# Kernel tuning notes

Measured on AMD Instinct MI355X. Metric: run time of the kernel, lower is better.

Reference implementation:

```python
import jax, jax.numpy as jnp
import numpy as np

P = 256          # planes == in_planes
EPS = 1e-5       # BatchNorm eps


def binarize(x):
    # sign with sign(0) -> +1, as in standard binary-net quantizers
    return jnp.where(x >= 0, 1.0, -1.0).astype(x.dtype)


def bin_conv(x, w, stride=1):
    """XNOR-style binarized 3x3 conv: sign(x) * sign(w), scaled by per-out-channel mean |w|."""
    ba = binarize(x)
    bw = binarize(w)
    scale = jnp.mean(jnp.abs(w), axis=(1, 2, 3))  # [O]
    y = jax.lax.conv_general_dilated(
        ba, bw, window_strides=(stride, stride), padding=((1, 1), (1, 1)),
        dimension_numbers=("NCHW", "OIHW", "NCHW"))
    return y * scale[None, :, None, None]


def bn(x, gamma, beta, mean, var):
    # inference-mode BatchNorm2d
    inv = gamma / jnp.sqrt(var + EPS)
    return x * inv[None, :, None, None] + (beta - mean * inv)[None, :, None, None]


def channel_shuffle(x, groups=2):
    b, c, h, w = x.shape
    return x.reshape(b, groups, c // groups, h, w).transpose(0, 2, 1, 3, 4).reshape(b, c, h, w)


def setup_inputs() -> dict:
    key = jax.random.key(0)
    ks = jax.random.split(key, 8)
    B, H, W = 16, 56, 56
    return {
        "x": jax.random.normal(ks[0], (B, 2 * P, H, W), jnp.float32),
        "w1": jax.random.normal(ks[1], (P, P, 3, 3), jnp.float32) * 0.05,
        "w2": jax.random.normal(ks[2], (P, 2 * P, 3, 3), jnp.float32) * 0.05,
        "gamma1": jnp.ones((P,), jnp.float32),
        "beta1": jnp.zeros((P,), jnp.float32),
        "mean1": jax.random.normal(ks[3], (P,), jnp.float32) * 0.1,
        "var1": jax.random.uniform(ks[4], (P,), jnp.float32) + 0.5,
        "gamma2": jnp.ones((P,), jnp.float32),
        "beta2": jnp.zeros((P,), jnp.float32),
        "mean2": jax.random.normal(ks[5], (P,), jnp.float32) * 0.1,
        "var2": jax.random.uniform(ks[6], (P,), jnp.float32) + 0.5,
        "move_bias": jax.random.normal(ks[7], (1, P, 1, 1), jnp.float32) * 0.1,
    }


def reference(x, w1, w2, gamma1, beta1, mean1, var1,
              gamma2, beta2, mean2, var2, move_bias):
    x_act, x_idle = x[:, :P], x[:, P:]
    residual = x_act
    out = bn(bin_conv(x_act, w1, stride=1), gamma1, beta1, mean1, var1)
    out = out + residual
    out = jnp.clip(out, -1.0, 1.0)            # Hardtanh
    x_idle = x_idle + move_bias               # LearnableBias
    out = jnp.concatenate([out, x_idle], axis=1)   # [B, 2P, H, W]
    out = channel_shuffle(out, groups=2)
    residual1 = out[:, :P]
    out = bn(bin_conv(out, w2, stride=1), gamma2, beta2, mean2, var2)
    out = out + residual1
    out = jnp.clip(out, -1.0, 1.0)            # Hardtanh
    return out
```

## Files before the change

### kernel.cpp

```cpp
#include <hip/hip_runtime.h>
#include <cstdint>

typedef unsigned long long u64;
typedef unsigned short u16;

#define HWSZ 3136
#define WD 56
#define NPIX 50176
#define HS 58
#define IMG 3364

__device__ __forceinline__ float clampf(float v){ return fminf(1.0f, fmaxf(-1.0f, v)); }
__device__ __forceinline__ u16 f2bf(float f){
    unsigned u = __float_as_uint(f);
    return (u16)((u + 0x7fffu + ((u >> 16) & 1u)) >> 16);
}
__device__ __forceinline__ float bf2f(u16 h){ return __uint_as_float(((unsigned)h) << 16); }
__device__ __forceinline__ int xp(u64 a, u64 b, int s){
    u64 x = a ^ b;
    s += __popc((unsigned)x);
    s += __popc((unsigned)(x >> 32));
    return s;
}

__device__ __forceinline__ void conv_pass2(
    const u64* __restrict__ bits, const u64* wlds, int colbase,
    int base, int (&accA)[8][2], int (&accB)[8][2])
{
#pragma unroll 1
    for (int dy = -1; dy <= 1; dy++) {
        const ulonglong2* rp = (const ulonglong2*)(bits + (size_t)(base + dy * HS) * 4);
        ulonglong2 plo[4], phi[4];
#pragma unroll
        for (int k = 0; k < 4; k++) { plo[k] = rp[2 * k]; phi[k] = rp[2 * k + 1]; }
#pragma unroll
        for (int dx = 0; dx < 3; dx++) {
            int t = (dy + 1) * 3 + dx;
#pragma unroll
            for (int co = 0; co < 8; co++) {
                const ulonglong2* wp = (const ulonglong2*)&wlds[((colbase + co) * 9 + t) * 4];
                ulonglong2 wA = wp[0], wB = wp[1];
#pragma unroll
                for (int p = 0; p < 2; p++) {
                    int k = dx + p; int s = accA[co][p];
                    s = xp(plo[k].x, wA.x, s); s = xp(plo[k].y, wA.y, s);
                    s = xp(phi[k].x, wB.x, s); s = xp(phi[k].y, wB.y, s);
                    accA[co][p] = s;
                }
            }
#pragma unroll
            for (int co = 0; co < 8; co++) {
                const ulonglong2* wp = (const ulonglong2*)&wlds[((colbase + 8 + co) * 9 + t) * 4];
                ulonglong2 wA = wp[0], wB = wp[1];
#pragma unroll
                for (int p = 0; p < 2; p++) {
                    int k = dx + p; int s = accB[co][p];
                    s = xp(plo[k].x, wA.x, s); s = xp(plo[k].y, wA.y, s);
                    s = xp(phi[k].x, wB.x, s); s = xp(phi[k].y, wB.y, s);
                    accB[co][p] = s;
                }
            }
        }
    }
}

__global__ __launch_bounds__(256) void k_wprep(
    const float* __restrict__ w1, const float* __restrict__ w2,
    const float* __restrict__ g1, const float* __restrict__ be1,
    const float* __restrict__ m1, const float* __restrict__ v1,
    const float* __restrict__ g2, const float* __restrict__ be2,
    const float* __restrict__ m2, const float* __restrict__ v2,
    u64* __restrict__ w1b, u64* __restrict__ w2e, u64* __restrict__ w2o,
    float* __restrict__ A1, float* __restrict__ B1,
    float* __restrict__ A2, float* __restrict__ B2,
    int* __restrict__ C1s, int* __restrict__ C2s)
{
    int co  = blockIdx.x;
    int tid = threadIdx.x;
    int wv = tid >> 6, lane = tid & 63;
    int ci = (wv << 6) + lane;

    __shared__ int spc1[4][9], spc2[4][9];

    float s1 = 0.f, s2 = 0.f;
    const float* w1p = w1 + ((size_t)co * 256 + ci) * 9;
#pragma unroll
    for (int t = 0; t < 9; t++) {
        float v = w1p[t];
        s1 += fabsf(v);
        u64 bal = __ballot(v >= 0.f);
        if (lane == 0) { w1b[(co * 9 + t) * 4 + wv] = bal; spc1[wv][t] = __popcll(bal); }
    }
    const float* wep = w2 + ((size_t)co * 512 + 2 * ci) * 9;
    const float* wop = wep + 9;
#pragma unroll
    for (int t = 0; t < 9; t++) {
        float ve = wep[t], vo = wop[t];
        s2 += fabsf(ve) + fabsf(vo);
        u64 bale = __ballot(ve >= 0.f);
        u64 balo = __ballot(vo >= 0.f);
        if (lane == 0) {
            w2e[(co * 9 + t) * 4 + wv] = bale; w2o[(co * 9 + t) * 4 + wv] = balo;
            spc2[wv][t] = __popcll(bale) + __popcll(balo);
        }
    }
    __shared__ float red1[256], red2[256];
    red1[tid] = s1; red2[tid] = s2;
    __syncthreads();
    for (int off = 128; off > 0; off >>= 1) {
        if (tid < off) { red1[tid] += red1[tid + off]; red2[tid] += red2[tid + off]; }
        __syncthreads();
    }
    if (tid == 0) {
        float scale1 = red1[0] / 2304.f;
        float scale2 = red2[0] / 4608.f;
        float inv1 = g1[co] / sqrtf(v1[co] + 1e-5f);
        float inv2 = g2[co] / sqrtf(v2[co] + 1e-5f);
        A1[co] = scale1 * inv1;  B1[co] = be1[co] - m1[co] * inv1;
        A2[co] = scale2 * inv2;  B2[co] = be2[co] - m2[co] * inv2;
        int pc1[9], pc2[9];
#pragma unroll
        for (int t = 0; t < 9; t++) {
            pc1[t] = spc1[0][t] + spc1[1][t] + spc1[2][t] + spc1[3][t];
            pc2[t] = spc2[0][t] + spc2[1][t] + spc2[2][t] + spc2[3][t];
        }
        int* c1 = C1s + co * 8;
        c1[0] = pc1[0] + pc1[1] + pc1[2];
        c1[1] = pc1[6] + pc1[7] + pc1[8];
        c1[2] = pc1[0] + pc1[3] + pc1[6];
        c1[3] = pc1[2] + pc1[5] + pc1[8];
        c1[4] = pc1[0]; c1[5] = pc1[2]; c1[6] = pc1[6]; c1[7] = pc1[8];
        int* c2 = C2s + co * 8;
        c2[0] = pc2[0] + pc2[1] + pc2[2];
        c2[1] = pc2[6] + pc2[7] + pc2[8];
        c2[2] = pc2[0] + pc2[3] + pc2[6];
        c2[3] = pc2[2] + pc2[5] + pc2[8];
        c2[4] = pc2[0]; c2[5] = pc2[2]; c2[6] = pc2[6]; c2[7] = pc2[8];
    }
}

__global__ __launch_bounds__(256) void k_zero(ulonglong2* __restrict__ dst, int n)
{
    int i = blockIdx.x * 256 + threadIdx.x;
    if (i < n) { ulonglong2 z; z.x = 0; z.y = 0; dst[i] = z; }
}

__global__ __launch_bounds__(256) void k_pack(
    const float* __restrict__ x, const float* __restrict__ mb,
    u64* __restrict__ bitsA, u64* __restrict__ bitsI)
{
    int tid = threadIdx.x;
    int p = blockIdx.x * 256 + tid;
    int q = blockIdx.y;
    int b = p / HWSZ, hw = p % HWSZ;
    int h = hw / WD, w = hw % WD;
    const float* xa = x + ((size_t)(b * 512 + q * 64)) * HWSZ + hw;
    const float* xi = x + ((size_t)(b * 512 + 256 + q * 64)) * HWSZ + hw;
    const float* mbq = mb + q * 64;
    u64 wa = 0, wi = 0;
#pragma unroll 8
    for (int j = 0; j < 64; j++) {
        float va = xa[(size_t)j * HWSZ];
        float vi = xi[(size_t)j * HWSZ] + mbq[j];
        wa |= (u64)(va >= 0.f) << j;
        wi |= (u64)(vi >= 0.f) << j;
    }
    size_t pos = ((size_t)b * IMG + (h + 1) * HS + (w + 1)) * 4 + q;
    bitsA[pos] = wa;
    bitsI[pos] = wi;
}

__global__ __launch_bounds__(256, 4) void k_conv1(
    const float* __restrict__ x, const u64* __restrict__ bitsA,
    const u64* __restrict__ w1b, const float* __restrict__ A1,
    const float* __restrict__ B1, const int* __restrict__ C1s,
    u64* __restrict__ bitsC, u16* __restrict__ c1v)
{
    __shared__ __align__(16) u64 sw[2304];
    __shared__ float sA[64], sB[64];
    __shared__ int scr[512];
    __shared__ u16 spart[4][128];
    int tid = threadIdx.x, q = blockIdx.y, cobase = q * 64;
    {
        const u64* src = w1b + (size_t)cobase * 36;
#pragma unroll
        for (int i = 0; i < 9; i++) sw[tid + i * 256] = src[tid + i * 256];
        if (tid < 64) { sA[tid] = A1[cobase + tid]; sB[tid] = B1[cobase + tid]; }
        scr[tid] = C1s[cobase * 8 + tid];
        scr[tid + 256] = C1s[cobase * 8 + tid + 256];
    }
    __syncthreads();

    int wid = tid >> 6, lane = tid & 63;
    int gu = __builtin_amdgcn_readfirstlane(wid);
    int pix0 = blockIdx.x * 128 + lane * 2;
    int b = pix0 / HWSZ, hw = pix0 % HWSZ, h = hw / WD, w = hw % WD;
    int base = b * IMG + (h + 1) * HS + w;

    int accA[8][2] = {}, accB[8][2] = {};
    conv_pass2(bitsA, sw, gu << 4, base, accA, accB);

    int mt = (h == 0), mbo = (h == WD - 1);
    int wl = (w == 0), wr = (w == 54);
    int nvr = 3 - mt - mbo;
    int nv0 = nvr * (3 - wl), nv1 = nvr * (3 - wr);

    unsigned sb0 = 0, sb1 = 0;
    bool wrv = (q < 2);
#pragma unroll
    for (int half = 0; half < 2; half++)
#pragma unroll
    for (int co = 0; co < 8; co++) {
        int col = (gu << 4) + half * 8 + co;
        int coG = cobase + col, bit = half * 8 + co;
        float A = sA[col], Bc = sB[col];
        const int* cs = &scr[col * 8];
        int a0 = half ? accB[co][0] : accA[co][0];
        int a1 = half ? accB[co][1] : accA[co][1];
        int ctb = (mt ? cs[0] : 0) + (mbo ? cs[1] : 0);
        int corr0 = ctb + (wl ? (cs[2] - (mt ? cs[4] : 0) - (mbo ? cs[6] : 0)) : 0);
        int corr1 = ctb + (wr ? (cs[3] - (mt ? cs[5] : 0) - (mbo ? cs[7] : 0)) : 0);
        float2 xr = *(const float2*)(x + ((size_t)(b * 512 + coG)) * HWSZ + hw);
        float v0 = (float)((nv0 << 8) + 2 * (corr0 - a0)) * A + Bc + xr.x;
        float v1 = (float)((nv1 << 8) + 2 * (corr1 - a1)) * A + Bc + xr.y;
        sb0 |= (unsigned)(v0 >= 0.f) << bit;
        sb1 |= (unsigned)(v1 >= 0.f) << bit;
        if (wrv) {
            ushort2 st; st.x = f2bf(clampf(v0)); st.y = f2bf(clampf(v1));
            *(ushort2*)(c1v + (size_t)coG * NPIX + pix0) = st;
        }
    }
    spart[wid][lane * 2]     = (u16)sb0;
    spart[wid][lane * 2 + 1] = (u16)sb1;
    __syncthreads();
    if (wid == 0) {
#pragma unroll
        for (int p = 0; p < 2; p++) {
            int pi = lane * 2 + p;
            u64 word = (u64)spart[0][pi] | ((u64)spart[1][pi] << 16)
                     | ((u64)spart[2][pi] << 32) | ((u64)spart[3][pi] << 48);
            bitsC[(size_t)(base + 1 + p) * 4 + q] = word;
        }
    }
}

__global__ __launch_bounds__(256, 4) void k_conv2(
    const float* __restrict__ x, const float* __restrict__ mb,
    const u64* __restrict__ bitsC, const u64* __restrict__ bitsI,
    const u64* __restrict__ w2e, const u64* __restrict__ w2o,
    const float* __restrict__ A2, const float* __restrict__ B2,
    const int* __restrict__ C2s,
    const u16* __restrict__ c1v, float* __restrict__ out)
{
    __shared__ __align__(16) u64 se[2304], so[2304];
    __shared__ float sA[64], sB[64], sM[32];
    __shared__ int scr[512];
    int tid = threadIdx.x, q = blockIdx.y, cobase = q * 64;
    {
        const u64* srcE = w2e + (size_t)cobase * 36;
        const u64* srcO = w2o + (size_t)cobase * 36;
#pragma unroll
        for (int i = 0; i < 9; i++) { se[tid + i * 256] = srcE[tid + i * 256]; so[tid + i * 256] = srcO[tid + i * 256]; }
        if (tid < 64) { sA[tid] = A2[cobase + tid]; sB[tid] = B2[cobase + tid]; }
        if (tid >= 64 && tid < 96) sM[tid - 64] = mb[q * 32 + tid - 64];
        scr[tid] = C2s[cobase * 8 + tid];
        scr[tid + 256] = C2s[cobase * 8 + tid + 256];
    }
    __syncthreads();

    int wid = tid >> 6, lane = tid & 63;
    int gu = __builtin_amdgcn_readfirstlane(wid);
    int pix0 = blockIdx.x * 128 + lane * 2;
    int b = pix0 / HWSZ, hw = pix0 % HWSZ, h = hw / WD, w = hw % WD;
    int base = b * IMG + (h + 1) * HS + w;

    int accA[8][2] = {}, accB[8][2] = {};
    conv_pass2(bitsC, se, gu << 4, base, accA, accB);
    conv_pass2(bitsI, so, gu << 4, base, accA, accB);

    int mt = (h == 0), mbo = (h == WD - 1);
    int wl = (w == 0), wr = (w == 54);
    int nvr = 3 - mt - mbo;
    int nv0 = nvr * (3 - wl), nv1 = nvr * (3 - wr);

#pragma unroll
    for (int half = 0; half < 2; half++)
#pragma unroll
    for (int co = 0; co < 8; co++) {
        int col = (gu << 4) + half * 8 + co;
        int coG = cobase + col, cg2 = coG >> 1;
        float A = sA[col], Bc = sB[col];
        const int* cs = &scr[col * 8];
        int a0 = half ? accB[co][0] : accA[co][0];
        int a1 = half ? accB[co][1] : accA[co][1];
        int ctb = (mt ? cs[0] : 0) + (mbo ? cs[1] : 0);
        int corr0 = ctb + (wl ? (cs[2] - (mt ? cs[4] : 0) - (mbo ? cs[6] : 0)) : 0);
        int corr1 = ctb + (wr ? (cs[3] - (mt ? cs[5] : 0) - (mbo ? cs[7] : 0)) : 0);
        float r0, r1;
        if ((co & 1) == 0) {
            ushort2 cv = *(const ushort2*)(c1v + (size_t)cg2 * NPIX + pix0);
            r0 = bf2f(cv.x); r1 = bf2f(cv.y);
        } else {
            float2 xi = *(const float2*)(x + ((size_t)(b * 512 + 256 + cg2)) * HWSZ + hw);
            float mv = sM[col >> 1];
            r0 = xi.x + mv; r1 = xi.y + mv;
        }
        float2 ov;
        ov.x = clampf((float)((nv0 << 9) + 2 * (corr0 - a0)) * A + Bc + r0);
        ov.y = clampf((float)((nv1 << 9) + 2 * (corr1 - a1)) * A + Bc + r1);
        *(float2*)(out + ((size_t)(b * 256 + coG)) * HWSZ + hw) = ov;
    }
}

extern "C" void kernel_launch(void* const* d_in, const int* in_sizes, int n_in,
                              void* d_out, int out_size, void* d_ws, size_t ws_size,
                              hipStream_t stream)
{
    const float* x   = (const float*)d_in[0];
    const float* w1  = (const float*)d_in[1];
    const float* w2  = (const float*)d_in[2];
    const float* g1  = (const float*)d_in[3];
    const float* be1 = (const float*)d_in[4];
    const float* m1  = (const float*)d_in[5];
    const float* v1  = (const float*)d_in[6];
    const float* g2  = (const float*)d_in[7];
    const float* be2 = (const float*)d_in[8];
    const float* m2  = (const float*)d_in[9];
    const float* v2  = (const float*)d_in[10];
    const float* mb  = (const float*)d_in[11];

    char* ws = (char*)d_ws;
    u64* w1b = (u64*)ws; ws += 73728;
    u64* w2e = (u64*)ws; ws += 73728;
    u64* w2o = (u64*)ws; ws += 73728;
    float* A1 = (float*)ws; ws += 1024;
    float* B1 = (float*)ws; ws += 1024;
    float* A2 = (float*)ws; ws += 1024;
    float* B2 = (float*)ws; ws += 1024;
    int* C1s = (int*)ws; ws += 8192;
    int* C2s = (int*)ws; ws += 8192;
    u64* bitsA = (u64*)ws; ws += (size_t)16 * IMG * 4 * 8;
    u64* bitsI = (u64*)ws; ws += (size_t)16 * IMG * 4 * 8;
    u64* bitsC = (u64*)ws; ws += (size_t)16 * IMG * 4 * 8;
    u16* c1v = (u16*)ws; ws += (size_t)128 * NPIX * 2;

    int nzero2 = (int)(3 * (size_t)16 * IMG * 4 * 8 / 16);

    hipLaunchKernelGGL(k_wprep, dim3(256), dim3(256), 0, stream,
                       w1, w2, g1, be1, m1, v1, g2, be2, m2, v2,
                       w1b, w2e, w2o, A1, B1, A2, B2, C1s, C2s);
    hipLaunchKernelGGL(k_zero, dim3((nzero2 + 255) / 256), dim3(256), 0, stream,
                       (ulonglong2*)bitsA, nzero2);
    hipLaunchKernelGGL(k_pack, dim3(196, 4), dim3(256), 0, stream, x, mb, bitsA, bitsI);
    hipLaunchKernelGGL(k_conv1, dim3(392, 4), dim3(256), 0, stream,
                       x, bitsA, w1b, A1, B1, C1s, bitsC, c1v);
    hipLaunchKernelGGL(k_conv2, dim3(392, 4), dim3(256), 0, stream,
                       x, mb, bitsC, bitsI, w2e, w2o, A2, B2, C2s, c1v, (float*)d_out);
}
```

Baseline: 438.5 us.

## Reshape binary conv register tile to 8 channels by 4 pixels per thread

Both binary conv kernels change each thread's tile from 16 output channels by 2 pixels to 8 channels by 4 pixels. Each loaded input bit row is now reused across four pixels instead of two, and each block covers 32 channels over 256 pixels with twice as many blocks in y. The epilogue moves to float4/ushort4 accesses, and bitsC is written as 32-bit quarter-words from byte partials. The cost is that each weight read from LDS now serves fewer channels per pixel load, and the grid is reshaped, which changes occupancy.

```diff
diff --git a/kernel.cpp b/kernel.cpp
--- a/kernel.cpp
+++ b/kernel.cpp
@@ -2,7 +2,9 @@
 #include <cstdint>
 
 typedef unsigned long long u64;
+typedef unsigned int u32;
 typedef unsigned short u16;
+typedef unsigned char u8;
 
 #define HWSZ 3136
 #define WD 56
@@ -23,16 +25,16 @@
     return s;
 }
 
-__device__ __forceinline__ void conv_pass2(
+__device__ __forceinline__ void conv_pass84(
     const u64* __restrict__ bits, const u64* wlds, int colbase,
-    int base, int (&accA)[8][2], int (&accB)[8][2])
+    int base, int (&acc)[8][4])
 {
 #pragma unroll 1
     for (int dy = -1; dy <= 1; dy++) {
         const ulonglong2* rp = (const ulonglong2*)(bits + (size_t)(base + dy * HS) * 4);
-        ulonglong2 plo[4], phi[4];
-#pragma unroll
-        for (int k = 0; k < 4; k++) { plo[k] = rp[2 * k]; phi[k] = rp[2 * k + 1]; }
+        ulonglong2 plo[6], phi[6];
+#pragma unroll
+        for (int k = 0; k < 6; k++) { plo[k] = rp[2 * k]; phi[k] = rp[2 * k + 1]; }
 #pragma unroll
         for (int dx = 0; dx < 3; dx++) {
             int t = (dy + 1) * 3 + dx;
@@ -41,23 +43,11 @@
                 const ulonglong2* wp = (const ulonglong2*)&wlds[((colbase + co) * 9 + t) * 4];
                 ulonglong2 wA = wp[0], wB = wp[1];
 #pragma unroll
-                for (int p = 0; p < 2; p++) {
-                    int k = dx + p; int s = accA[co][p];
+                for (int p = 0; p < 4; p++) {
+                    int k = dx + p; int s = acc[co][p];
                     s = xp(plo[k].x, wA.x, s); s = xp(plo[k].y, wA.y, s);
                     s = xp(phi[k].x, wB.x, s); s = xp(phi[k].y, wB.y, s);
-                    accA[co][p] = s;
-                }
-            }
-#pragma unroll
-            for (int co = 0; co < 8; co++) {
-                const ulonglong2* wp = (const ulonglong2*)&wlds[((colbase + 8 + co) * 9 + t) * 4];
-                ulonglong2 wA = wp[0], wB = wp[1];
-#pragma unroll
-                for (int p = 0; p < 2; p++) {
-                    int k = dx + p; int s = accB[co][p];
-                    s = xp(plo[k].x, wA.x, s); s = xp(plo[k].y, wA.y, s);
-                    s = xp(phi[k].x, wB.x, s); s = xp(phi[k].y, wB.y, s);
-                    accB[co][p] = s;
+                    acc[co][p] = s;
                 }
             }
         }
@@ -174,72 +164,77 @@
     const float* __restrict__ x, const u64* __restrict__ bitsA,
     const u64* __restrict__ w1b, const float* __restrict__ A1,
     const float* __restrict__ B1, const int* __restrict__ C1s,
-    u64* __restrict__ bitsC, u16* __restrict__ c1v)
-{
-    __shared__ __align__(16) u64 sw[2304];
-    __shared__ float sA[64], sB[64];
-    __shared__ int scr[512];
-    __shared__ u16 spart[4][128];
-    int tid = threadIdx.x, q = blockIdx.y, cobase = q * 64;
+    u32* __restrict__ bitsC32, u16* __restrict__ c1v)
+{
+    __shared__ __align__(16) u64 sw[1152];
+    __shared__ float sA[32], sB[32];
+    __shared__ int scr[256];
+    __shared__ u8 spart[4][256];
+    int tid = threadIdx.x, y = blockIdx.y, cog = y * 32;
     {
-        const u64* src = w1b + (size_t)cobase * 36;
-#pragma unroll
-        for (int i = 0; i < 9; i++) sw[tid + i * 256] = src[tid + i * 256];
-        if (tid < 64) { sA[tid] = A1[cobase + tid]; sB[tid] = B1[cobase + tid]; }
-        scr[tid] = C1s[cobase * 8 + tid];
-        scr[tid + 256] = C1s[cobase * 8 + tid + 256];
+        const u64* src = w1b + (size_t)cog * 36;
+        for (int i = tid; i < 1152; i += 256) sw[i] = src[i];
+        if (tid < 32) { sA[tid] = A1[cog + tid]; sB[tid] = B1[cog + tid]; }
+        scr[tid] = C1s[cog * 8 + tid];
     }
     __syncthreads();
 
     int wid = tid >> 6, lane = tid & 63;
     int gu = __builtin_amdgcn_readfirstlane(wid);
-    int pix0 = blockIdx.x * 128 + lane * 2;
+    int pix0 = blockIdx.x * 256 + lane * 4;
     int b = pix0 / HWSZ, hw = pix0 % HWSZ, h = hw / WD, w = hw % WD;
     int base = b * IMG + (h + 1) * HS + w;
 
-    int accA[8][2] = {}, accB[8][2] = {};
-    conv_pass2(bitsA, sw, gu << 4, base, accA, accB);
+    int acc[8][4] = {};
+    conv_pass84(bitsA, sw, gu << 3, base, acc);
 
     int mt = (h == 0), mbo = (h == WD - 1);
-    int wl = (w == 0), wr = (w == 54);
+    int wl = (w == 0), wrr = (w == 52);
     int nvr = 3 - mt - mbo;
-    int nv0 = nvr * (3 - wl), nv1 = nvr * (3 - wr);
-
-    unsigned sb0 = 0, sb1 = 0;
-    bool wrv = (q < 2);
-#pragma unroll
-    for (int half = 0; half < 2; half++)
+    int nv[4];
+#pragma unroll
+    for (int p = 0; p < 4; p++) {
+        int wp_ = w + p;
+        nv[p] = nvr * (3 - (wp_ == 0) - (wp_ == WD - 1));
+    }
+
+    u32 sb[4] = {0, 0, 0, 0};
+    bool wrv = (y < 4);
 #pragma unroll
     for (int co = 0; co < 8; co++) {
-        int col = (gu << 4) + half * 8 + co;
-        int coG = cobase + col, bit = half * 8 + co;
+        int col = (gu << 3) + co;
+        int coG = cog + col;
         float A = sA[col], Bc = sB[col];
         const int* cs = &scr[col * 8];
-        int a0 = half ? accB[co][0] : accA[co][0];
-        int a1 = half ? accB[co][1] : accA[co][1];
         int ctb = (mt ? cs[0] : 0) + (mbo ? cs[1] : 0);
-        int corr0 = ctb + (wl ? (cs[2] - (mt ? cs[4] : 0) - (mbo ? cs[6] : 0)) : 0);
-        int corr1 = ctb + (wr ? (cs[3] - (mt ? cs[5] : 0) - (mbo ? cs[7] : 0)) : 0);
-        float2 xr = *(const float2*)(x + ((size_t)(b * 512 + coG)) * HWSZ + hw);
-        float v0 = (float)((nv0 << 8) + 2 * (corr0 - a0)) * A + Bc + xr.x;
-        float v1 = (float)((nv1 << 8) + 2 * (corr1 - a1)) * A + Bc + xr.y;
-        sb0 |= (unsigned)(v0 >= 0.f) << bit;
-        sb1 |= (unsigned)(v1 >= 0.f) << bit;
+        int L = wl  ? (cs[2] - (mt ? cs[4] : 0) - (mbo ? cs[6] : 0)) : 0;
+        int R = wrr ? (cs[3] - (mt ? cs[5] : 0) - (mbo ? cs[7] : 0)) : 0;
+        float4 xr = *(const float4*)(x + ((size_t)(b * 512 + coG)) * HWSZ + hw);
+        float v0 = (float)((nv[0] << 8) + 2 * (ctb + L - acc[co][0])) * A + Bc + xr.x;
+        float v1 = (float)((nv[1] << 8) + 2 * (ctb     - acc[co][1])) * A + Bc + xr.y;
+        float v2 = (float)((nv[2] << 8) + 2 * (ctb     - acc[co][2])) * A + Bc + xr.z;
+        float v3 = (float)((nv[3] << 8) + 2 * (ctb + R - acc[co][3])) * A + Bc + xr.w;
+        sb[0] |= (u32)(v0 >= 0.f) << co;
+        sb[1] |= (u32)(v1 >= 0.f) << co;
+        sb[2] |= (u32)(v2 >= 0.f) << co;
+        sb[3] |= (u32)(v3 >= 0.f) << co;
         if (wrv) {
-            ushort2 st; st.x = f2bf(clampf(v0)); st.y = f2bf(clampf(v1));
-            *(ushort2*)(c1v + (size_t)coG * NPIX + pix0) = st;
-        }
-    }
-    spart[wid][lane * 2]     = (u16)sb0;
-    spart[wid][lane * 2 + 1] = (u16)sb1;
+            ushort4 st;
+            st.x = f2bf(clampf(v0)); st.y = f2bf(clampf(v1));
+            st.z = f2bf(clampf(v2)); st.w = f2bf(clampf(v3));
+            *(ushort4*)(c1v + (size_t)coG * NPIX + pix0) = st;
+        }
+    }
+#pragma unroll
+    for (int p = 0; p < 4; p++) spart[wid][lane * 4 + p] = (u8)sb[p];
     __syncthreads();
     if (wid == 0) {
 #pragma unroll
-        for (int p = 0; p < 2; p++) {
-            int pi = lane * 2 + p;
-            u64 word = (u64)spart[0][pi] | ((u64)spart[1][pi] << 16)
-                     | ((u64)spart[2][pi] << 32) | ((u64)spart[3][pi] << 48);
-            bitsC[(size_t)(base + 1 + p) * 4 + q] = word;
+        for (int p = 0; p < 4; p++) {
+            int pi = lane * 4 + p;
+            u32 word = (u32)spart[0][pi] | ((u32)spart[1][pi] << 8)
+                     | ((u32)spart[2][pi] << 16) | ((u32)spart[3][pi] << 24);
+            bitsC32[(size_t)(base + 1 + p) * 8 + y] = word;
         }
     }
 }
@@ -252,63 +247,64 @@
     const int* __restrict__ C2s,
     const u16* __restrict__ c1v, float* __restrict__ out)
 {
-    __shared__ __align__(16) u64 se[2304], so[2304];
-    __shared__ float sA[64], sB[64], sM[32];
-    __shared__ int scr[512];
-    int tid = threadIdx.x, q = blockIdx.y, cobase = q * 64;
+    __shared__ __align__(16) u64 se[1152], so[1152];
+    __shared__ float sA[32], sB[32], sM[16];
+    __shared__ int scr[256];
+    int tid = threadIdx.x, y = blockIdx.y, cog = y * 32;
     {
-        const u64* srcE = w2e + (size_t)cobase * 36;
-        const u64* srcO = w2o + (size_t)cobase * 36;
-#pragma unroll
-        for (int i = 0; i < 9; i++) { se[tid + i * 256] = srcE[tid + i * 256]; so[tid + i * 256] = srcO[tid + i * 256]; }
-        if (tid < 64) { sA[tid] = A2[cobase + tid]; sB[tid] = B2[cobase + tid]; }
-        if (tid >= 64 && tid < 96) sM[tid - 64] = mb[q * 32 + tid - 64];
-        scr[tid] = C2s[cobase * 8 + tid];
-        scr[tid + 256] = C2s[cobase * 8 + tid + 256];
+        const u64* srcE = w2e + (size_t)cog * 36;
+        const u64* srcO = w2o + (size_t)cog * 36;
+        for (int i = tid; i < 1152; i += 256) { se[i] = srcE[i]; so[i] = srcO[i]; }
+        if (tid < 32) { sA[tid] = A2[cog + tid]; sB[tid] = B2[cog + tid]; }
+        if (tid >= 32 && tid < 48) sM[tid - 32] = mb[cog / 2 + tid - 32];
+        scr[tid] = C2s[cog * 8 + tid];
     }
     __syncthreads();
 
     int wid = tid >> 6, lane = tid & 63;
     int gu = __builtin_amdgcn_readfirstlane(wid);
-    int pix0 = blockIdx.x * 128 + lane * 2;
+    int pix0 = blockIdx.x * 256 + lane * 4;
     int b = pix0 / HWSZ, hw = pix0 % HWSZ, h = hw / WD, w = hw % WD;
     int base = b * IMG + (h + 1) * HS + w;
 
-    int accA[8][2] = {}, accB[8][2] = {};
-    conv_pass2(bitsC, se, gu << 4, base, accA, accB);
-    conv_pass2(bitsI, so, gu << 4, base, accA, accB);
+    int acc[8][4] = {};
+    conv_pass84(bitsC, se, gu << 3, base, acc);
+    conv_pass84(bitsI, so, gu << 3, base, acc);
 
     int mt = (h == 0), mbo = (h == WD - 1);
-    int wl = (w == 0), wr = (w == 54);
+    int wl = (w == 0), wrr = (w == 52);
     int nvr = 3 - mt - mbo;
-    int nv0 = nvr * (3 - wl), nv1 = nvr * (3 - wr);
-
-#pragma unroll
-    for (int half = 0; half < 2; half++)
+    int nv[4];
+#pragma unroll
+    for (int p = 0; p < 4; p++) {
+        int wp_ = w + p;
+        nv[p] = nvr * (3 - (wp_ == 0) - (wp_ == WD - 1));
+    }
+
 #pragma unroll
     for (int co = 0; co < 8; co++) {
-        int col = (gu << 4) + half * 8 + co;
-        int coG = cobase + col, cg2 = coG >> 1;
+        int col = (gu << 3) + co;
+        int coG = cog + col, cg2 = coG >> 1;
         float A = sA[col], Bc = sB[col];
         const int* cs = &scr[col * 8];
-        int a0 = half ? accB[co][0] : accA[co][0];
-        int a1 = half ? accB[co][1] : accA[co][1];
         int ctb = (mt ? cs[0] : 0) + (mbo ? cs[1] : 0);
-        int corr0 = ctb + (wl ? (cs[2] - (mt ? cs[4] : 0) - (mbo ? cs[6] : 0)) : 0);
-        int corr1 = ctb + (wr ? (cs[3] - (mt ? cs[5] : 0) - (mbo ? cs[7] : 0)) : 0);
-        float r0, r1;
-        if ((co & 1) == 0) {
-            ushort2 cv = *(const ushort2*)(c1v + (size_t)cg2 * NPIX + pix0);
-            r0 = bf2f(cv.x); r1 = bf2f(cv.y);
+        int L = wl  ? (cs[2] - (mt ? cs[4] : 0) - (mbo ? cs[6] : 0)) : 0;
+        int R = wrr ? (cs[3] - (mt ? cs[5] : 0) - (mbo ? cs[7] : 0)) : 0;
+        float r0, r1, r2, r3;
+        if ((col & 1) == 0) {
+            ushort4 cv = *(const ushort4*)(c1v + (size_t)cg2 * NPIX + pix0);
+            r0 = bf2f(cv.x); r1 = bf2f(cv.y); r2 = bf2f(cv.z); r3 = bf2f(cv.w);
         } else {
-            float2 xi = *(const float2*)(x + ((size_t)(b * 512 + 256 + cg2)) * HWSZ + hw);
+            float4 xi = *(const float4*)(x + ((size_t)(b * 512 + 256 + cg2)) * HWSZ + hw);
             float mv = sM[col >> 1];
-            r0 = xi.x + mv; r1 = xi.y + mv;
-        }
-        float2 ov;
-        ov.x = clampf((float)((nv0 << 9) + 2 * (corr0 - a0)) * A + Bc + r0);
-        ov.y = clampf((float)((nv1 << 9) + 2 * (corr1 - a1)) * A + Bc + r1);
-        *(float2*)(out + ((size_t)(b * 256 + coG)) * HWSZ + hw) = ov;
+            r0 = xi.x + mv; r1 = xi.y + mv; r2 = xi.z + mv; r3 = xi.w + mv;
+        }
+        float4 ov;
+        ov.x = clampf((float)((nv[0] << 9) + 2 * (ctb + L - acc[co][0])) * A + Bc + r0);
+        ov.y = clampf((float)((nv[1] << 9) + 2 * (ctb     - acc[co][1])) * A + Bc + r1);
+        ov.z = clampf((float)((nv[2] << 9) + 2 * (ctb     - acc[co][2])) * A + Bc + r2);
+        ov.w = clampf((float)((nv[3] << 9) + 2 * (ctb + R - acc[co][3])) * A + Bc + r3);
+        *(float4*)(out + ((size_t)(b * 256 + coG)) * HWSZ + hw) = ov;
     }
 }
 
@@ -352,8 +348,8 @@
     hipLaunchKernelGGL(k_zero, dim3((nzero2 + 255) / 256), dim3(256), 0, stream,
                        (ulonglong2*)bitsA, nzero2);
     hipLaunchKernelGGL(k_pack, dim3(196, 4), dim3(256), 0, stream, x, mb, bitsA, bitsI);
-    hipLaunchKernelGGL(k_conv1, dim3(392, 4), dim3(256), 0, stream,
-                       x, bitsA, w1b, A1, B1, C1s, bitsC, c1v);
-    hipLaunchKernelGGL(k_conv2, dim3(392, 4), dim3(256), 0, stream,
+    hipLaunchKernelGGL(k_conv1, dim3(196, 8), dim3(256), 0, stream,
+                       x, bitsA, w1b, A1, B1, C1s, (u32*)bitsC, c1v);
+    hipLaunchKernelGGL(k_conv2, dim3(196, 8), dim3(256), 0, stream,
                        x, mb, bitsC, bitsI, w2e, w2o, A2, B2, C2s, c1v, (float*)d_out);
 }
```

New measurement: 436.5 us. No clear change (-0.5%).
